# Performance work log

Hardware: AMD Instinct MI355X
Metric: run time of the kernel (lower is better)

The kernel has to match this reference:

```python
import jax, jax.numpy as jnp
import numpy as np

B, C, T = 8, 512, 4096
KC, VC, H = 512, 512, 1  # key_channels, value_channels, num_heads
SCALE = KC // (H ** 0.5)  # faithful to original: key_channels // num_heads**0.5


def setup_inputs() -> dict:
    key = jax.random.key(0)
    k1, k2, k3, k4, k5 = jax.random.split(key, 5)
    x = jax.random.normal(k1, (B, C, T), dtype=jnp.float32)
    # 1x1 Conv1d weights: Conv1d(C, out, kernel_size=1) == per-timestep Linear
    Wqk = jax.random.normal(k2, (KC, C), dtype=jnp.float32) / np.sqrt(C)
    bqk = jax.random.normal(k3, (KC,), dtype=jnp.float32) * 0.01
    Wv = jax.random.normal(k4, (VC, C), dtype=jnp.float32) / np.sqrt(C)
    bv = jax.random.normal(k5, (VC,), dtype=jnp.float32) * 0.01
    return {"x": x, "Wqk": Wqk, "bqk": bqk, "Wv": Wv, "bv": bv}


def reference(x, Wqk, bqk, Wv, bv):
    # 1x1 conv projections: [B,C,T] -> [B,K,T] / [B,V,T]
    qk = jnp.einsum('kc,bct->bkt', Wqk, x) + bqk[None, :, None]
    val = jnp.einsum('vc,bct->bvt', Wv, x) + bv[None, :, None]
    # channel-wise attention: with num_heads=1 the reshape/transpose/matmul
    # chain reduces to scores[b,k,v] = sum_t qk[b,k,t] * val[b,v,t]
    scores = jnp.einsum('bkt,bvt->bkv', qk, val) / SCALE
    p = jax.nn.softmax(scores, axis=-1)          # softmax over value channels
    # inference path: dropout is identity (self.training == False)
    out = jnp.einsum('bkv,bvt->bkt', p, val)     # [B,K,T], K == input_channels
    return out.reshape(-1, C, T)
```

## Files before the change

kernel.cpp:

```cpp
#include <hip/hip_runtime.h>
#include <hip/hip_bf16.h>


#define BB 8
#define CC 512
#define TT 4096

typedef __attribute__((ext_vector_type(8))) short bf16x8;
typedef __attribute__((ext_vector_type(4))) short bf16x4;
typedef __attribute__((ext_vector_type(4))) float f32x4;

__device__ __forceinline__ void gload_lds16(const void* g, void* l) {
  __builtin_amdgcn_global_load_lds((const __attribute__((address_space(1))) void*)g,
                                   (__attribute__((address_space(3))) void*)l,
                                   16, 0, 0);
}
__device__ __forceinline__ float bf2f(short u) {
  return __uint_as_float(((unsigned)(unsigned short)u) << 16);
}
__device__ __forceinline__ unsigned short f2bf(float f) {
  return __builtin_bit_cast(unsigned short, __float2bfloat16(f));
}

__global__ __launch_bounds__(256)
void convert_stream_kernel(const float* __restrict__ x, __hip_bfloat16* __restrict__ xh,
                           float* __restrict__ sx)
{
  const int gid = blockIdx.x * 256 + threadIdx.x;
#pragma unroll
  for (int it = 0; it < 4; it++) {
    const int chunk = it * 524288 + gid;
    const size_t base = (size_t)chunk * 8;
    const float4 a = *(const float4*)&x[base];
    const float4 c = *(const float4*)&x[base + 4];
    bf16x8 h;
    h[0] = (short)f2bf(a.x); h[1] = (short)f2bf(a.y);
    h[2] = (short)f2bf(a.z); h[3] = (short)f2bf(a.w);
    h[4] = (short)f2bf(c.x); h[5] = (short)f2bf(c.y);
    h[6] = (short)f2bf(c.z); h[7] = (short)f2bf(c.w);
    *(bf16x8*)&xh[base] = h;
    float s = ((a.x + a.y) + (a.z + a.w)) + ((c.x + c.y) + (c.z + c.w));
#pragma unroll
    for (int off = 32; off; off >>= 1) s += __shfl_xor(s, off);
    if ((threadIdx.x & 63) == 0) atomicAdd(&sx[chunk >> 9], s);
  }
}

__global__ __launch_bounds__(256)
void prep_w_kernel(const float* __restrict__ Wqk, const float* __restrict__ Wv,
                   const float* __restrict__ sx,
                   __hip_bfloat16* __restrict__ Wqkh, __hip_bfloat16* __restrict__ Wvh,
                   __hip_bfloat16* __restrict__ WvT,
                   float* __restrict__ ta, float* __restrict__ tb)
{
  const int blk = blockIdx.x;
  if (blk < 1024) {
    int i = blk * 256 + threadIdx.x;
    Wqkh[i] = __float2bfloat16(Wqk[i]);
    float wv = Wv[i];
    Wvh[i] = __float2bfloat16(wv);
    WvT[(i & 511) * 512 + (i >> 9)] = __float2bfloat16(wv);
  } else {
    int wid = threadIdx.x >> 6, lane = threadIdx.x & 63;
    int gid = (blk - 1024) * 4 + wid;
    int which = gid >> 12;
    int rem = gid & 4095;
    int b = rem >> 9, j = rem & 511;
    const float* W = which ? Wv : Wqk;
    float s = 0.f;
#pragma unroll
    for (int i2 = 0; i2 < 8; i2++) {
      int c = lane + i2 * 64;
      s += W[j * 512 + c] * sx[b * 512 + c];
    }
#pragma unroll
    for (int off = 32; off; off >>= 1) s += __shfl_xor(s, off);
    if (lane == 0) (which ? tb : ta)[b * 512 + j] = s;
  }
}

template <int BM, int BN, int EPI>
__global__ __launch_bounds__(256)
void gemm_nt_kernel(const __hip_bfloat16* __restrict__ A, long strideA, int ldA,
                    const __hip_bfloat16* __restrict__ B, long strideB, int ldB,
                    void* __restrict__ C, long strideC, int ldC,
                    int Kslice, int nslices)
{
  constexpr int FM = BM / 32, FN = BN / 32;
  const int tid = threadIdx.x, lane = tid & 63, wid = tid >> 6;

  const int gx = gridDim.x, gy = gridDim.y;
  const int lin = blockIdx.x + gx * (blockIdx.y + gy * blockIdx.z);
  const int nwg = gx * gy * (int)gridDim.z;
  const int lin2 = (lin & 7) * (nwg >> 3) + (lin >> 3);
  const int tn = lin2 % gx;
  const int r1 = lin2 / gx;
  const int tm = r1 % gy;
  const int z  = r1 / gy;
  const int b  = z / nslices;
  const int ks = z - b * nslices;

  const __hip_bfloat16* Ab = A + (size_t)b * strideA + (size_t)(tm * BM) * ldA + (size_t)ks * Kslice;
  const __hip_bfloat16* Bb = B + (size_t)b * strideB + (size_t)(tn * BN) * ldB + (size_t)ks * Kslice;

  __shared__ __align__(16) __hip_bfloat16 sA[2][BM * 64];
  __shared__ __align__(16) __hip_bfloat16 sB[2][BN * 64];

  const int wr = wid >> 1, wc = wid & 1;

  f32x4 acc[FM][FN];
#pragma unroll
  for (int m = 0; m < FM; m++)
#pragma unroll
    for (int n = 0; n < FN; n++) acc[m][n] = (f32x4){0.f, 0.f, 0.f, 0.f};

  auto stage = [&](int buf, int k0) {
#pragma unroll
    for (int i = 0; i < BM / 32; i++) {
      int e = tid * 8 + i * 2048;
      int row = e >> 6, colg = (e & 63) ^ ((row & 7) << 3);
      gload_lds16(Ab + (size_t)row * ldA + k0 + colg, &sA[buf][wid * 512 + i * 2048]);
    }
#pragma unroll
    for (int i = 0; i < BN / 32; i++) {
      int e = tid * 8 + i * 2048;
      int row = e >> 6, colg = (e & 63) ^ ((row & 7) << 3);
      gload_lds16(Bb + (size_t)row * ldB + k0 + colg, &sB[buf][wid * 512 + i * 2048]);
    }
  };

  stage(0, 0);
  __syncthreads();
  const int nsteps = Kslice >> 6;
  for (int s = 0; s < nsteps; s++) {
    if (s + 1 < nsteps) stage((s + 1) & 1, (s + 1) << 6);
    const __hip_bfloat16* cA = sA[s & 1];
    const __hip_bfloat16* cB = sB[s & 1];
#pragma unroll
    for (int ks2 = 0; ks2 < 2; ks2++) {
      bf16x8 af[FM], bfv[FN];
      const int kb = ks2 * 32 + (lane >> 4) * 8;
#pragma unroll
      for (int m = 0; m < FM; m++) {
        int row = wr * (BM / 2) + m * 16 + (lane & 15);
        af[m] = *(const bf16x8*)&cA[row * 64 + (kb ^ ((row & 7) << 3))];
      }
#pragma unroll
      for (int n = 0; n < FN; n++) {
        int row = wc * (BN / 2) + n * 16 + (lane & 15);
        bfv[n] = *(const bf16x8*)&cB[row * 64 + (kb ^ ((row & 7) << 3))];
      }
#pragma unroll
      for (int m = 0; m < FM; m++)
#pragma unroll
        for (int n = 0; n < FN; n++)
          acc[m][n] = __builtin_amdgcn_mfma_f32_16x16x32_bf16(af[m], bfv[n], acc[m][n], 0, 0, 0);
    }
    __syncthreads();
  }

  const int rb = tm * BM + wr * (BM / 2) + ((lane >> 4) << 2);
  const int cb = tn * BN + wc * (BN / 2) + (lane & 15);
  __hip_bfloat16* Cb = (__hip_bfloat16*)C + (size_t)z * strideC;
#pragma unroll
  for (int m = 0; m < FM; m++)
#pragma unroll
    for (int n = 0; n < FN; n++)
#pragma unroll
      for (int r = 0; r < 4; r++) {
        int row = rb + m * 16 + r, col = cb + n * 16;
        Cb[(size_t)row * ldC + col] = __float2bfloat16(acc[m][n][r]);
      }
}

__global__ __launch_bounds__(256)
void reduce_g_kernel(const short* __restrict__ Gpart, short* __restrict__ Gb)
{
  const int idx = (blockIdx.x * 256 + threadIdx.x) * 8;
  const int b = idx >> 18, i = idx & 262143;
  const short* base = Gpart + ((size_t)(b * 4) << 18) + i;
  float s[8];
#pragma unroll
  for (int q = 0; q < 8; q++) s[q] = 0.f;
#pragma unroll
  for (int ks = 0; ks < 4; ks++) {
    bf16x8 v = *(const bf16x8*)(base + ((size_t)ks << 18));
#pragma unroll
    for (int q = 0; q < 8; q++) s[q] += bf2f(v[q]);
  }
  bf16x8 o;
#pragma unroll
  for (int q = 0; q < 8; q++) o[q] = (short)f2bf(s[q]);
  *(bf16x8*)(Gb + ((size_t)b << 18) + i) = o;
}

__global__ __launch_bounds__(256)
void middle_kernel(const __hip_bfloat16* __restrict__ Gh,
                   const __hip_bfloat16* __restrict__ Wqkh,
                   const __hip_bfloat16* __restrict__ Wvh,
                   const __hip_bfloat16* __restrict__ WvT,
                   const float* __restrict__ bqk, const float* __restrict__ bv,
                   const float* __restrict__ ta, const float* __restrict__ tb,
                   __hip_bfloat16* __restrict__ Mm, float* __restrict__ pb)
{
  __shared__ __align__(16) __hip_bfloat16 sW[16 * 512];
  __shared__ __align__(16) __hip_bfloat16 sT[16 * 512];
  __shared__ __align__(16) __hip_bfloat16 sB[2][512 * 32];
  __shared__ float red1[4][16], red2[4][16], red3[4][16];

  const int tid = threadIdx.x, lane = tid & 63, wid = tid >> 6;
  const int lin = blockIdx.x;
  const int lin2 = (lin & 7) * 32 + (lin >> 3);
  const int strip = lin2 & 31, b = lin2 >> 5;
  const __hip_bfloat16* Ghb = Gh + (size_t)b * 262144;

#pragma unroll
  for (int i = 0; i < 4; i++) {
    int row = i * 4 + wid;
    int scol = 8 * (lane ^ (row & 7));
    gload_lds16(Wqkh + (size_t)(strip * 16 + row) * 512 + scol, &sW[i * 2048 + wid * 512]);
  }

  auto stageB = [&](int buf, const __hip_bfloat16* Bsrc, int k0) {
#pragma unroll
    for (int i = 0; i < 8; i++) {
      int r = i * 64 + wid * 16 + (lane >> 2);
      int scol = k0 + 8 * ((lane & 3) ^ (r & 3));
      gload_lds16(Bsrc + (size_t)r * 512 + scol, &sB[buf][i * 2048 + wid * 512]);
    }
  };

  const int arow = lane & 15;
  const int asw = (arow & 7) << 3;
  f32x4 acc[8];

#define RUN_STAGE(BSRC, SX)                                                     \
  {                                                                             \
    _Pragma("unroll") for (int n = 0; n < 8; n++) acc[n] = (f32x4){0.f,0.f,0.f,0.f}; \
    stageB(0, BSRC, 0);                                                         \
    __syncthreads();                                                            \
    for (int t = 0; t < 16; t++) {                                              \
      if (t < 15) stageB((t + 1) & 1, BSRC, (t + 1) * 32);                      \
      const __hip_bfloat16* cB = sB[t & 1];                                     \
      const int kq = t * 32 + (lane >> 4) * 8;                                  \
      bf16x8 af = *(const bf16x8*)&SX[arow * 512 + (kq ^ asw)];                 \
      const int kb = (lane >> 4) * 8;                                           \
      _Pragma("unroll") for (int n = 0; n < 8; n++) {                           \
        int brow = wid * 128 + n * 16 + (lane & 15);                            \
        bf16x8 bfv = *(const bf16x8*)&cB[brow * 32 + (kb ^ ((brow & 3) << 3))]; \
        acc[n] = __builtin_amdgcn_mfma_f32_16x16x32_bf16(af, bfv, acc[n], 0, 0, 0); \
      }                                                                         \
      __syncthreads();                                                          \
    }                                                                           \
  }

  RUN_STAGE(Ghb, sW);
#pragma unroll
  for (int n = 0; n < 8; n++)
#pragma unroll
    for (int r = 0; r < 4; r++) {
      int lr = ((lane >> 4) << 2) + r;
      int col = wid * 128 + n * 16 + (lane & 15);
      sT[lr * 512 + (col ^ ((lr & 7) << 3))] = __float2bfloat16(acc[n][r]);
    }
  __syncthreads();

  RUN_STAGE(Wvh, sT);

  const float* tab = ta + b * 512;
  const float* tbb = tb + b * 512;
  float bvc[8], tbc[8];
#pragma unroll
  for (int n = 0; n < 8; n++) {
    int col = wid * 128 + n * 16 + (lane & 15);
    bvc[n] = bv[col]; tbc[n] = tbb[col];
  }
  float bq[4], tar[4];
#pragma unroll
  for (int r = 0; r < 4; r++) {
    int gr = strip * 16 + ((lane >> 4) << 2) + r;
    bq[r] = bqk[gr]; tar[r] = tab[gr];
  }
#pragma unroll
  for (int n = 0; n < 8; n++)
#pragma unroll
    for (int r = 0; r < 4; r++)
      acc[n][r] = (acc[n][r] + bq[r] * tbc[n] + tar[r] * bvc[n]
                   + 4096.0f * bq[r] * bvc[n]) * (1.0f / 512.0f);

#pragma unroll
  for (int r = 0; r < 4; r++) {
    float v = acc[0][r];
#pragma unroll
    for (int n = 1; n < 8; n++) v = fmaxf(v, acc[n][r]);
#pragma unroll
    for (int off = 1; off < 16; off <<= 1) v = fmaxf(v, __shfl_xor(v, off));
    if ((lane & 15) == 0) red1[wid][((lane >> 4) << 2) + r] = v;
  }
  __syncthreads();
  float mx[4];
#pragma unroll
  for (int r = 0; r < 4; r++) {
    int lr = ((lane >> 4) << 2) + r;
    mx[r] = fmaxf(fmaxf(red1[0][lr], red1[1][lr]), fmaxf(red1[2][lr], red1[3][lr]));
  }
#pragma unroll
  for (int r = 0; r < 4; r++) {
    float s = 0.f, pp = 0.f;
#pragma unroll
    for (int n = 0; n < 8; n++) {
      float e = __expf(acc[n][r] - mx[r]);
      acc[n][r] = e;
      s += e; pp += e * bvc[n];
    }
#pragma unroll
    for (int off = 1; off < 16; off <<= 1) { s += __shfl_xor(s, off); pp += __shfl_xor(pp, off); }
    if ((lane & 15) == 0) {
      red2[wid][((lane >> 4) << 2) + r] = s;
      red3[wid][((lane >> 4) << 2) + r] = pp;
    }
  }
  __syncthreads();
  float inv[4];
#pragma unroll
  for (int r = 0; r < 4; r++) {
    int lr = ((lane >> 4) << 2) + r;
    float sum = red2[0][lr] + red2[1][lr] + red2[2][lr] + red2[3][lr];
    inv[r] = 1.0f / sum;
    if (wid == 0 && (lane & 15) == 0)
      pb[b * 512 + strip * 16 + lr] =
          (red3[0][lr] + red3[1][lr] + red3[2][lr] + red3[3][lr]) * inv[r];
  }
#pragma unroll
  for (int n = 0; n < 8; n++)
#pragma unroll
    for (int r = 0; r < 4; r++) {
      int lr = ((lane >> 4) << 2) + r;
      int col = wid * 128 + n * 16 + (lane & 15);
      sT[lr * 512 + (col ^ ((lr & 7) << 3))] = __float2bfloat16(acc[n][r] * inv[r]);
    }
  __syncthreads();

  RUN_STAGE(WvT, sT);
#undef RUN_STAGE

  __hip_bfloat16* Mb = Mm + (size_t)b * 262144 + (size_t)(strip * 16) * 512;
#pragma unroll
  for (int n = 0; n < 8; n++)
#pragma unroll
    for (int r = 0; r < 4; r++) {
      int lr = ((lane >> 4) << 2) + r;
      int col = wid * 128 + n * 16 + (lane & 15);
      Mb[(size_t)lr * 512 + col] = __float2bfloat16(acc[n][r]);
    }
}

__global__ __launch_bounds__(256)
void gemm_out_kernel(const __hip_bfloat16* __restrict__ Mall,
                     const __hip_bfloat16* __restrict__ xh,
                     const float* __restrict__ pball,
                     float* __restrict__ out)
{
  __shared__ __align__(16) __hip_bfloat16 sA[2][128 * 64];
  __shared__ __align__(16) __hip_bfloat16 sB[2][64 * 128];

  const int tid = threadIdx.x, lane = tid & 63, wid = tid >> 6;
  const int wr = wid >> 1, wc = wid & 1;

  const int lin = blockIdx.x + 32 * (blockIdx.y + 4 * blockIdx.z);
  const int lin2 = (lin & 7) * 128 + (lin >> 3);
  const int tm = lin2 & 3;
  const int tn = (lin2 >> 2) & 31;
  const int b  = lin2 >> 7;

  const __hip_bfloat16* Ab = Mall + (size_t)b * 262144 + (size_t)(tm * 128) * 512;
  const __hip_bfloat16* Bb = xh + (size_t)b * ((size_t)CC * TT) + tn * 128;

  f32x4 acc[4][4];
#pragma unroll
  for (int m = 0; m < 4; m++)
#pragma unroll
    for (int n = 0; n < 4; n++) acc[m][n] = (f32x4){0.f, 0.f, 0.f, 0.f};

  auto stage = [&](int buf, int k0) {
#pragma unroll
    for (int i = 0; i < 4; i++) {
      int e = tid * 8 + i * 2048;
      int row = e >> 6, colg = (e & 63) ^ ((row & 7) << 3);
      gload_lds16(Ab + (size_t)row * 512 + k0 + colg, &sA[buf][wid * 512 + i * 2048]);
    }
#pragma unroll
    for (int q = 0; q < 4; q++) {
      int E = q * 2048 + tid * 8;
      int v = ((E >> 9) << 2) | ((E >> 4) & 3);
      int t = (((E >> 6) & 7) << 4) | (E & 8);
      gload_lds16(Bb + (size_t)(k0 + v) * TT + t, &sB[buf][wid * 512 + q * 2048]);
    }
  };

  const unsigned sB32 =
      (unsigned)(size_t)(__attribute__((address_space(3))) __hip_bfloat16*)&sB[0][0];
  const unsigned btr_lo = sB32 + (lane >> 4) * 2048 + (lane & 15) * 8 + wc * 512;
  const unsigned btr_hi = btr_lo + 8192;

#define COMPUTE(BUF)                                                            \
  {                                                                             \
    _Pragma("unroll")                                                           \
    for (int ks2 = 0; ks2 < 2; ks2++) {                                         \
      bf16x8 af[4]; bf16x4 blo[4], bhi[4];                                      \
      const int kb = ks2 * 32 + (lane >> 4) * 8;                                \
      _Pragma("unroll")                                                         \
      for (int m = 0; m < 4; m++) {                                             \
        int row = wr * 64 + m * 16 + (lane & 15);                               \
        af[m] = *(const bf16x8*)&sA[BUF][row * 64 + (kb ^ ((row & 7) << 3))];   \
      }                                                                         \
      unsigned ab = ks2 ? btr_hi : btr_lo;                                      \
      _Pragma("unroll")                                                         \
      for (int n = 0; n < 4; n++) {                                             \
        asm volatile("ds_read_b64_tr_b16 %0, %1 offset:%2"                      \
                     : "=v"(blo[n]) : "v"(ab), "i"((BUF) * 16384 + n * 128));   \
        asm volatile("ds_read_b64_tr_b16 %0, %1 offset:%2"                      \
                     : "=v"(bhi[n]) : "v"(ab), "i"((BUF) * 16384 + n * 128 + 1024)); \
      }                                                                         \
      asm volatile("s_waitcnt lgkmcnt(0)" ::: "memory");                        \
      __builtin_amdgcn_sched_barrier(0);                                        \
      _Pragma("unroll")                                                         \
      for (int m = 0; m < 4; m++)                                               \
        _Pragma("unroll")                                                       \
        for (int n = 0; n < 4; n++) {                                           \
          bf16x8 b8 = __builtin_shufflevector(blo[n], bhi[n], 0, 1, 2, 3, 4, 5, 6, 7); \
          acc[m][n] = __builtin_amdgcn_mfma_f32_16x16x32_bf16(af[m], b8, acc[m][n], 0, 0, 0); \
        }                                                                       \
    }                                                                           \
  }

  stage(0, 0);
  __syncthreads();
#pragma unroll 1
  for (int s = 0; s < 8; s += 2) {
    if (s + 1 < 8) stage(1, (s + 1) * 64);
    COMPUTE(0);
    __syncthreads();
    if (s + 2 < 8) stage(0, (s + 2) * 64);
    COMPUTE(1);
    __syncthreads();
  }
#undef COMPUTE

  const int rb = tm * 128 + wr * 64 + ((lane >> 4) << 2);
  const int cb = tn * 128 + wc * 64 + (lane & 15);
  float* Cf = out + (size_t)b * ((size_t)CC * TT);
  const float* pbv = pball + b * 512;
#pragma unroll
  for (int m = 0; m < 4; m++)
#pragma unroll
    for (int n = 0; n < 4; n++)
#pragma unroll
      for (int r = 0; r < 4; r++) {
        int row = rb + m * 16 + r, col = cb + n * 16;
        Cf[(size_t)row * TT + col] = acc[m][n][r] + pbv[row];
      }
}

extern "C" void kernel_launch(void* const* d_in, const int* in_sizes, int n_in,
                              void* d_out, int out_size, void* d_ws, size_t ws_size,
                              hipStream_t stream)
{
  const float* x   = (const float*)d_in[0];
  const float* Wqk = (const float*)d_in[1];
  const float* bqk = (const float*)d_in[2];
  const float* Wv  = (const float*)d_in[3];
  const float* bv  = (const float*)d_in[4];
  float* out = (float*)d_out;

  char* w = (char*)d_ws;
  auto alloc = [&](size_t bytes) {
    void* pp = (void*)w;
    w += (bytes + 255) & ~(size_t)255;
    return pp;
  };
  __hip_bfloat16* xh     = (__hip_bfloat16*)alloc((size_t)BB * CC * TT * 2);
  short*          Gpart  = (short*)alloc((size_t)BB * 4 * CC * CC * 2);
  short*          Gb     = (short*)alloc((size_t)BB * CC * CC * 2);
  __hip_bfloat16* Mm     = (__hip_bfloat16*)alloc((size_t)BB * CC * CC * 2);
  __hip_bfloat16* Wqkh   = (__hip_bfloat16*)alloc((size_t)CC * CC * 2);
  __hip_bfloat16* Wvh    = (__hip_bfloat16*)alloc((size_t)CC * CC * 2);
  __hip_bfloat16* WvT    = (__hip_bfloat16*)alloc((size_t)CC * CC * 2);
  float* sx = (float*)alloc((size_t)BB * CC * 4);
  float* ta = (float*)alloc((size_t)BB * CC * 4);
  float* tb = (float*)alloc((size_t)BB * CC * 4);
  float* pb = (float*)alloc((size_t)BB * CC * 4);

  hipMemsetAsync(sx, 0, (size_t)BB * CC * 4, stream);

  convert_stream_kernel<<<2048, 256, 0, stream>>>(x, xh, sx);
  prep_w_kernel<<<3072, 256, 0, stream>>>(Wqk, Wv, sx, Wqkh, Wvh, WvT, ta, tb);

  const long sXH = (long)CC * TT;
  const long sSq = (long)CC * CC;

  gemm_nt_kernel<128, 128, 0><<<dim3(4, 4, BB * 4), 256, 0, stream>>>(
      xh, sXH, TT, xh, sXH, TT, Gpart, sSq, CC, 1024, 4);
  reduce_g_kernel<<<(BB * CC * CC) / (256 * 8), 256, 0, stream>>>(Gpart, Gb);

  middle_kernel<<<256, 256, 0, stream>>>(
      (const __hip_bfloat16*)Gb, Wqkh, Wvh, WvT, bqk, bv, ta, tb, Mm, pb);

  gemm_out_kernel<<<dim3(32, 4, 8), 256, 0, stream>>>(Mm, xh, pb, out);
}
```

Baseline: 220.1 us.

## Prefetch two stages ahead with vmcnt-counted waits instead of full syncthreads

Replaces __syncthreads-based double buffering in the three GEMM-style kernels with a two-deep prefetch. Each kernel issues loads for stages s+1 and s+2, waits with s_waitcnt vmcnt(8) so only the current stage's global-to-LDS loads must finish, and uses bare s_barrier fences. The middle kernel also chains its three 16-step stages into one continuous 48-tile pipeline and changes the LDS swizzle for its B tile. The aim is to hide global load latency behind MFMA work and avoid draining all outstanding loads at each barrier, with correctness now depending on hand-counted load numbers.

```diff
diff --git a/kernel.cpp b/kernel.cpp
--- a/kernel.cpp
+++ b/kernel.cpp
@@ -20,6 +20,16 @@
 }
 __device__ __forceinline__ unsigned short f2bf(float f) {
   return __builtin_bit_cast(unsigned short, __float2bfloat16(f));
+}
+__device__ __forceinline__ void bar_fence() {
+  asm volatile("" ::: "memory");
+  __builtin_amdgcn_s_barrier();
+  asm volatile("" ::: "memory");
+}
+__device__ __forceinline__ void bar_lds() {
+  asm volatile("s_waitcnt lgkmcnt(0)" ::: "memory");
+  __builtin_amdgcn_s_barrier();
+  asm volatile("" ::: "memory");
 }
 
 __global__ __launch_bounds__(256)
@@ -79,13 +89,14 @@
   }
 }
 
-template <int BM, int BN, int EPI>
+template <int BM, int BN>
 __global__ __launch_bounds__(256)
 void gemm_nt_kernel(const __hip_bfloat16* __restrict__ A, long strideA, int ldA,
                     const __hip_bfloat16* __restrict__ B, long strideB, int ldB,
                     void* __restrict__ C, long strideC, int ldC,
                     int Kslice, int nslices)
 {
+  static_assert(BM == 128 && BN == 128, "vmcnt(8) count assumes 8 loads/stage");
   constexpr int FM = BM / 32, FN = BN / 32;
   const int tid = threadIdx.x, lane = tid & 63, wid = tid >> 6;
 
@@ -129,11 +140,14 @@
     }
   };
 
+  const int nsteps = Kslice >> 6;
   stage(0, 0);
-  __syncthreads();
-  const int nsteps = Kslice >> 6;
+  if (nsteps > 1) stage(1, 64);
+#pragma unroll 1
   for (int s = 0; s < nsteps; s++) {
-    if (s + 1 < nsteps) stage((s + 1) & 1, (s + 1) << 6);
+    if (s + 1 < nsteps) asm volatile("s_waitcnt vmcnt(8)" ::: "memory");
+    else                asm volatile("s_waitcnt vmcnt(0)" ::: "memory");
+    bar_fence();
     const __hip_bfloat16* cA = sA[s & 1];
     const __hip_bfloat16* cB = sB[s & 1];
 #pragma unroll
@@ -156,7 +170,8 @@
         for (int n = 0; n < FN; n++)
           acc[m][n] = __builtin_amdgcn_mfma_f32_16x16x32_bf16(af[m], bfv[n], acc[m][n], 0, 0, 0);
     }
-    __syncthreads();
+    bar_fence();
+    if (s + 2 < nsteps) stage(s & 1, (s + 2) << 6);
   }
 
   const int rb = tm * BM + wr * (BM / 2) + ((lane >> 4) << 2);
@@ -221,40 +236,49 @@
     gload_lds16(Wqkh + (size_t)(strip * 16 + row) * 512 + scol, &sW[i * 2048 + wid * 512]);
   }
 
-  auto stageB = [&](int buf, const __hip_bfloat16* Bsrc, int k0) {
+  auto stageB = [&](int buf, int gt) {
+    const __hip_bfloat16* Bsrc = (gt < 16) ? Ghb : (gt < 32 ? Wvh : WvT);
+    const int k0 = (gt & 15) * 32;
 #pragma unroll
     for (int i = 0; i < 8; i++) {
       int r = i * 64 + wid * 16 + (lane >> 2);
-      int scol = k0 + 8 * ((lane & 3) ^ (r & 3));
+      int scol = k0 + 8 * ((lane & 3) ^ ((r >> 1) & 3));
       gload_lds16(Bsrc + (size_t)r * 512 + scol, &sB[buf][i * 2048 + wid * 512]);
     }
   };
+
+  stageB(0, 0);
+  stageB(1, 1);
 
   const int arow = lane & 15;
   const int asw = (arow & 7) << 3;
+  const int kb = (lane >> 4) * 8;
   f32x4 acc[8];
 
-#define RUN_STAGE(BSRC, SX)                                                     \
-  {                                                                             \
-    _Pragma("unroll") for (int n = 0; n < 8; n++) acc[n] = (f32x4){0.f,0.f,0.f,0.f}; \
-    stageB(0, BSRC, 0);                                                         \
-    __syncthreads();                                                            \
-    for (int t = 0; t < 16; t++) {                                              \
-      if (t < 15) stageB((t + 1) & 1, BSRC, (t + 1) * 32);                      \
-      const __hip_bfloat16* cB = sB[t & 1];                                     \
-      const int kq = t * 32 + (lane >> 4) * 8;                                  \
-      bf16x8 af = *(const bf16x8*)&SX[arow * 512 + (kq ^ asw)];                 \
-      const int kb = (lane >> 4) * 8;                                           \
-      _Pragma("unroll") for (int n = 0; n < 8; n++) {                           \
-        int brow = wid * 128 + n * 16 + (lane & 15);                            \
-        bf16x8 bfv = *(const bf16x8*)&cB[brow * 32 + (kb ^ ((brow & 3) << 3))]; \
-        acc[n] = __builtin_amdgcn_mfma_f32_16x16x32_bf16(af, bfv, acc[n], 0, 0, 0); \
-      }                                                                         \
-      __syncthreads();                                                          \
-    }                                                                           \
-  }
-
-  RUN_STAGE(Ghb, sW);
+  auto run16 = [&](int base, const __hip_bfloat16* SX) {
+#pragma unroll
+    for (int n = 0; n < 8; n++) acc[n] = (f32x4){0.f, 0.f, 0.f, 0.f};
+#pragma unroll 1
+    for (int t = 0; t < 16; t++) {
+      const int gt = base + t;
+      if (gt + 1 < 48) asm volatile("s_waitcnt vmcnt(8)" ::: "memory");
+      else             asm volatile("s_waitcnt vmcnt(0)" ::: "memory");
+      bar_fence();
+      const __hip_bfloat16* cB = sB[gt & 1];
+      const int kq = t * 32 + kb;
+      bf16x8 af = *(const bf16x8*)&SX[arow * 512 + (kq ^ asw)];
+#pragma unroll
+      for (int n = 0; n < 8; n++) {
+        int brow = wid * 128 + n * 16 + (lane & 15);
+        bf16x8 bfv = *(const bf16x8*)&cB[brow * 32 + (kb ^ (((brow >> 1) & 3) << 3))];
+        acc[n] = __builtin_amdgcn_mfma_f32_16x16x32_bf16(af, bfv, acc[n], 0, 0, 0);
+      }
+      bar_fence();
+      if (gt + 2 < 48) stageB(gt & 1, gt + 2);
+    }
+  };
+
+  run16(0, sW);
 #pragma unroll
   for (int n = 0; n < 8; n++)
 #pragma unroll
@@ -263,9 +287,9 @@
       int col = wid * 128 + n * 16 + (lane & 15);
       sT[lr * 512 + (col ^ ((lr & 7) << 3))] = __float2bfloat16(acc[n][r]);
     }
-  __syncthreads();
-
-  RUN_STAGE(Wvh, sT);
+  bar_lds();
+
+  run16(16, sT);
 
   const float* tab = ta + b * 512;
   const float* tbb = tb + b * 512;
@@ -297,7 +321,7 @@
     for (int off = 1; off < 16; off <<= 1) v = fmaxf(v, __shfl_xor(v, off));
     if ((lane & 15) == 0) red1[wid][((lane >> 4) << 2) + r] = v;
   }
-  __syncthreads();
+  bar_lds();
   float mx[4];
 #pragma unroll
   for (int r = 0; r < 4; r++) {
@@ -320,7 +344,7 @@
       red3[wid][((lane >> 4) << 2) + r] = pp;
     }
   }
-  __syncthreads();
+  bar_lds();
   float inv[4];
 #pragma unroll
   for (int r = 0; r < 4; r++) {
@@ -339,10 +363,9 @@
       int col = wid * 128 + n * 16 + (lane & 15);
       sT[lr * 512 + (col ^ ((lr & 7) << 3))] = __float2bfloat16(acc[n][r] * inv[r]);
     }
-  __syncthreads();
-
-  RUN_STAGE(WvT, sT);
-#undef RUN_STAGE
+  bar_lds();
+
+  run16(32, sT);
 
   __hip_bfloat16* Mb = Mm + (size_t)b * 262144 + (size_t)(strip * 16) * 512;
 #pragma unroll
@@ -435,15 +458,20 @@
   }
 
   stage(0, 0);
-  __syncthreads();
+  stage(1, 64);
 #pragma unroll 1
   for (int s = 0; s < 8; s += 2) {
-    if (s + 1 < 8) stage(1, (s + 1) * 64);
+    asm volatile("s_waitcnt vmcnt(8)" ::: "memory");
+    bar_fence();
     COMPUTE(0);
-    __syncthreads();
+    bar_fence();
     if (s + 2 < 8) stage(0, (s + 2) * 64);
+    if (s + 2 < 8) asm volatile("s_waitcnt vmcnt(8)" ::: "memory");
+    else           asm volatile("s_waitcnt vmcnt(0)" ::: "memory");
+    bar_fence();
     COMPUTE(1);
-    __syncthreads();
+    bar_fence();
+    if (s + 3 < 8) stage(1, (s + 3) * 64);
   }
 #undef COMPUTE
 
@@ -499,7 +527,7 @@
   const long sXH = (long)CC * TT;
   const long sSq = (long)CC * CC;
 
-  gemm_nt_kernel<128, 128, 0><<<dim3(4, 4, BB * 4), 256, 0, stream>>>(
+  gemm_nt_kernel<128, 128><<<dim3(4, 4, BB * 4), 256, 0, stream>>>(
       xh, sXH, TT, xh, sXH, TT, Gpart, sSq, CC, 1024, 4);
   reduce_g_kernel<<<(BB * CC * CC) / (256 * 8), 256, 0, stream>>>(Gpart, Gb);
 
```

Measured after the change: 215.7 us. 2.0% less time.
